# Optimization experiments

Measured on AMD Instinct MI355X. Metric: run time of the kernel, lower is better.

Reference implementation:

```python
import jax, jax.numpy as jnp
import numpy as np


def setup_inputs() -> dict:
    key = jax.random.key(0)
    ks = jax.random.split(key, 8)
    B, C, H, W, D = 2, 128, 16, 16, 16
    C8 = C // 8
    return {
        "x": jax.random.normal(ks[0], (B, C, H, W, D), dtype=jnp.float32),
        "wq": jax.random.normal(ks[1], (C8, C), dtype=jnp.float32) * (1.0 / np.sqrt(C)),
        "bq": jax.random.normal(ks[2], (C8,), dtype=jnp.float32) * 0.02,
        "wk": jax.random.normal(ks[3], (C8, C), dtype=jnp.float32) * (1.0 / np.sqrt(C)),
        "bk": jax.random.normal(ks[4], (C8,), dtype=jnp.float32) * 0.02,
        "wv": jax.random.normal(ks[5], (C, C), dtype=jnp.float32) * (1.0 / np.sqrt(C)),
        "bv": jax.random.normal(ks[6], (C,), dtype=jnp.float32) * 0.02,
        "gamma": jax.random.normal(ks[7], (1,), dtype=jnp.float32) * 0.1,
    }


def reference(x, wq, bq, wk, bk, wv, bv, gamma):
    B, C, H, W, D = x.shape
    N = H * W * D
    xf = x.reshape(B, C, N)                      # (B, C, N) flatten H,W,D
    # 1x1x1 convs == per-voxel linear over channels
    q = jnp.einsum('oc,bcn->bon', wq, xf) + bq[None, :, None]   # (B, C//8, N)
    k = jnp.einsum('oc,bcn->bon', wk, xf) + bk[None, :, None]   # (B, C//8, N)
    v = jnp.einsum('oc,bcn->bon', wv, xf) + bv[None, :, None]   # (B, C, N)
    # energy[b, i, j] = sum_c q[b,c,i] * k[b,c,j]  (no scaling, as in source)
    energy = jnp.einsum('bci,bcj->bij', q, k)                   # (B, N, N)
    attn = jax.nn.softmax(energy, axis=-1)
    # out[b,c,i] = sum_j v[b,c,j] * attn[b,i,j]
    out = jnp.einsum('bcj,bij->bci', v, attn)                   # (B, C, N)
    out = out.reshape(B, C, H, W, D)
    return gamma[0] * out + x
```

## Files before the change

kernel.cpp:

```cpp
#include <hip/hip_runtime.h>
#include <hip/hip_bf16.h>
#include <math.h>

#define N_VOX 4096
#define LOG2E 1.44269504f

typedef __bf16 bf16x4 __attribute__((ext_vector_type(4)));
typedef __bf16 bf16x8 __attribute__((ext_vector_type(8)));
typedef float f32x4 __attribute__((ext_vector_type(4)));
typedef float f32x16 __attribute__((ext_vector_type(16)));

#define QT_OFF 0
#define KT_OFF 262144
#define VP_OFF 524288

__device__ __forceinline__ f32x16 mfma32_bf16(bf16x8 a, bf16x8 b, f32x16 c) {
  return __builtin_amdgcn_mfma_f32_32x32x16_bf16(a, b, c, 0, 0, 0);
}
__device__ __forceinline__ f32x16 mfma32_fp8(long a, long b, f32x16 c) {
  return __builtin_amdgcn_mfma_f32_32x32x16_fp8_fp8(a, b, c, 0, 0, 0);
}
__device__ __forceinline__ void pinl(long& v) { asm volatile("" : "+v"(v)); }
__device__ __forceinline__ void pinb(bf16x8& v) { asm volatile("" : "+v"(v)); }

__device__ __forceinline__ unsigned f32_to_fp8x4(float a, float b, float c, float d) {
  int v = __builtin_amdgcn_cvt_pk_fp8_f32(a, b, 0, false);
  v = __builtin_amdgcn_cvt_pk_fp8_f32(c, d, v, true);
  return (unsigned)v;
}
__device__ __forceinline__ unsigned char f32_to_fp8(float a) {
  return (unsigned char)(__builtin_amdgcn_cvt_pk_fp8_f32(a, a, 0, false) & 0xff);
}

__global__ __launch_bounds__(256) void proj_kernel(
    const float* __restrict__ x,
    const float* __restrict__ wq, const float* __restrict__ bq,
    const float* __restrict__ wk, const float* __restrict__ bk,
    const float* __restrict__ wv, const float* __restrict__ bv,
    unsigned char* __restrict__ ws8) {
  __shared__ __bf16 xs[32 * 136];
  __shared__ __bf16 wb[160 * 136];

  const int t   = threadIdx.x;
  const int bid = blockIdx.x;
  const int b   = bid >> 7;
  const int n0  = (bid & 127) * 32;

  for (int i = t; i < 5120; i += 256) {
    int gid = i * 4;
    const float* src = (gid < 2048) ? wq + gid
                     : (gid < 4096) ? wk + (gid - 2048)
                                    : wv + (gid - 4096);
    float4 f = *reinterpret_cast<const float4*>(src);
    int r = gid >> 7, col = gid & 127;
    bf16x4 o;
    o[0] = (__bf16)f.x; o[1] = (__bf16)f.y; o[2] = (__bf16)f.z; o[3] = (__bf16)f.w;
    *reinterpret_cast<bf16x4*>(&wb[r * 136 + col]) = o;
  }
  for (int idx = t; idx < 128 * 8; idx += 256) {
    int c = idx >> 3, v4 = idx & 7;
    float4 xv = *reinterpret_cast<const float4*>(
        x + (size_t)(b * 128 + c) * N_VOX + n0 + v4 * 4);
    xs[(v4 * 4 + 0) * 136 + c] = (__bf16)xv.x;
    xs[(v4 * 4 + 1) * 136 + c] = (__bf16)xv.y;
    xs[(v4 * 4 + 2) * 136 + c] = (__bf16)xv.z;
    xs[(v4 * 4 + 3) * 136 + c] = (__bf16)xv.w;
  }
  __syncthreads();

  const int w = t >> 6, lane = t & 63;
  const int cq = lane & 15, g = lane >> 4, g8 = g * 8, g4 = g * 4;

  __bf16* qt = reinterpret_cast<__bf16*>(ws8 + QT_OFF);
  __bf16* kt = reinterpret_cast<__bf16*>(ws8 + KT_OFF);
  unsigned char* vp = ws8 + VP_OFF;
  const f32x4 zero4 = {0.f, 0.f, 0.f, 0.f};

  for (int ot = w; ot < 10; ot += 4) {
    int wrow = (ot == 0) ? cq : (ot == 1) ? 16 + cq : 32 + (ot - 2) * 16 + cq;
    const float* bias = (ot == 0) ? bq : (ot == 1) ? bk : bv + (ot - 2) * 16;

    f32x4 acc[2] = {zero4, zero4};
#pragma unroll
    for (int ks = 0; ks < 4; ++ks) {
      bf16x8 af = *reinterpret_cast<const bf16x8*>(&wb[wrow * 136 + ks * 32 + g8]);
#pragma unroll
      for (int nf = 0; nf < 2; ++nf) {
        bf16x8 bfr = *reinterpret_cast<const bf16x8*>(
            &xs[(nf * 16 + cq) * 136 + ks * 32 + g8]);
        acc[nf] = __builtin_amdgcn_mfma_f32_16x16x32_bf16(af, bfr, acc[nf], 0, 0, 0);
      }
    }

    float4 bl = *reinterpret_cast<const float4*>(bias + g4);
    const float* blp = reinterpret_cast<const float*>(&bl);
#pragma unroll
    for (int nf = 0; nf < 2; ++nf) {
      int n = n0 + nf * 16 + cq;
      if (ot < 2) {
        bf16x4 pk;
#pragma unroll
        for (int v = 0; v < 4; ++v) {
          float val = acc[nf][v] + blp[v];
          pk[v] = (__bf16)((ot == 0) ? val * LOG2E : val);
        }
        __bf16* dst = (ot == 0) ? qt : kt;
        *reinterpret_cast<bf16x4*>(dst + (size_t)(b * 4096 + n) * 16 + g4) = pk;
      } else {
#pragma unroll
        for (int v = 0; v < 4; ++v) {
          float val = acc[nf][v] + blp[v];
          int c = (ot - 2) * 16 + g4 + v;
          vp[(((size_t)(b * 256 + (n >> 4)) * 2 + (c >> 6)) << 10)
             + (((((n >> 3) & 1) << 5) | (c & 31)) * 16)
             + ((c >> 5) & 1) * 8 + (n & 7)] = f32_to_fp8(val);
        }
      }
    }
  }
}

__global__ __launch_bounds__(512, 2) void attn_kernel(
    const unsigned char* __restrict__ ws8,
    const float* __restrict__ x,
    const float* __restrict__ gamma_p,
    float* __restrict__ out) {
  __shared__ float o_lds[4][128][33];
  __shared__ float m_lds[8][32], l_lds[8][32], lstar_lds[32];

  const int t    = threadIdx.x;
  const int w    = t >> 6;
  const int lane = t & 63;
  const int l31  = lane & 31;
  const int hi   = lane >> 5;

  const int raw = blockIdx.x;
  const int xcd = raw & 7;
  const int b   = xcd >> 2;
  const int qt0 = ((raw >> 3) * 4 + (xcd & 3)) * 32;

  const __bf16* qt = reinterpret_cast<const __bf16*>(ws8 + QT_OFF);
  const __bf16* kt = reinterpret_cast<const __bf16*>(ws8 + KT_OFF);
  const unsigned char* vp = ws8 + VP_OFF;

  bf16x8 qf = *reinterpret_cast<const bf16x8*>(
      qt + (size_t)(b * 4096 + qt0 + l31) * 16 + hi * 8);

  f32x16 acc[4];
#pragma unroll
  for (int cb = 0; cb < 4; ++cb)
#pragma unroll
    for (int r = 0; r < 16; ++r) acc[cb][r] = 0.f;
  const f32x16 zero16 = acc[0];
  float m = -1e30f, l = 0.f;

  const __bf16* kbase = kt + (size_t)(b * 4096 + l31) * 16 + hi * 8;
  const unsigned char* vbase = vp + (size_t)b * 524288 + lane * 16;

  const int jt_base = w * 8;

  bf16x8 kf0 = *reinterpret_cast<const bf16x8*>(kbase + (size_t)(jt_base * 64) * 16);
  bf16x8 kf1 = *reinterpret_cast<const bf16x8*>(kbase + (size_t)(jt_base * 64 + 32) * 16);

#pragma unroll 1
  for (int tile = 0; tile < 8; ++tile) {
    const int jt = jt_base + tile;
    const int jtn = jt_base + ((tile + 1) & 7);

    long vf[4][4];
#pragma unroll
    for (int jc = 0; jc < 4; ++jc)
#pragma unroll
      for (int ch = 0; ch < 2; ++ch) {
        long2 L = *reinterpret_cast<const long2*>(
            vbase + (((size_t)(jt * 4 + jc) * 2 + ch) << 10));
        vf[jc][2 * ch] = L.x; vf[jc][2 * ch + 1] = L.y;
      }
    bf16x8 kn0 = *reinterpret_cast<const bf16x8*>(kbase + (size_t)(jtn * 64) * 16);
    bf16x8 kn1 = *reinterpret_cast<const bf16x8*>(kbase + (size_t)(jtn * 64 + 32) * 16);

    f32x16 sf0 = mfma32_bf16(kf0, qf, zero16);
    f32x16 sf1 = mfma32_bf16(kf1, qf, zero16);

    float tmax = sf0[0];
#pragma unroll
    for (int r = 1; r < 16; ++r) tmax = fmaxf(tmax, sf0[r]);
#pragma unroll
    for (int r = 0; r < 16; ++r) tmax = fmaxf(tmax, sf1[r]);
    tmax = fmaxf(tmax, __shfl_xor(tmax, 32));

    if (__any(tmax > m + 8.0f)) {
      float mn = fmaxf(m, tmax);
      float sc = exp2f(m - mn);
#pragma unroll
      for (int cb = 0; cb < 4; ++cb)
#pragma unroll
        for (int r = 0; r < 16; ++r) acc[cb][r] *= sc;
      l *= sc;
      m = mn;
    }

    float psum = 0.f;
    unsigned W0[4], W1[4], X0[4], X1[4];
#pragma unroll
    for (int i = 0; i < 4; ++i) {
      float a = exp2f(sf0[4 * i] - m),     bb = exp2f(sf0[4 * i + 1] - m);
      float c = exp2f(sf0[4 * i + 2] - m), d  = exp2f(sf0[4 * i + 3] - m);
      psum += (a + bb) + (c + d);
      W0[i] = f32_to_fp8x4(a, bb, c, d);
    }
#pragma unroll
    for (int i = 0; i < 4; ++i) {
      float a = exp2f(sf1[4 * i] - m),     bb = exp2f(sf1[4 * i + 1] - m);
      float c = exp2f(sf1[4 * i + 2] - m), d  = exp2f(sf1[4 * i + 3] - m);
      psum += (a + bb) + (c + d);
      W1[i] = f32_to_fp8x4(a, bb, c, d);
    }
    psum += __shfl_xor(psum, 32);
    l += psum;

#pragma unroll
    for (int i = 0; i < 4; ++i) {
      X0[i] = __shfl_xor(W0[i], 32);
      X1[i] = __shfl_xor(W1[i], 32);
    }

#pragma unroll
    for (int jc = 0; jc < 4; ++jc)
#pragma unroll
      for (int cb = 0; cb < 4; ++cb) pinl(vf[jc][cb]);
    pinb(kn0); pinb(kn1);

    __builtin_amdgcn_s_setprio(1);
#pragma unroll
    for (int jc = 0; jc < 4; ++jc) {
      const int pb = (jc & 1) * 2;
      unsigned wd0, wd1;
      if (jc < 2) {
        wd0 = hi ? X0[pb + 1] : W0[pb];
        wd1 = hi ? W0[pb + 1] : X0[pb];
      } else {
        wd0 = hi ? X1[pb + 1] : W1[pb];
        wd1 = hi ? W1[pb + 1] : X1[pb];
      }
      long pf = (long)(((unsigned long long)wd1 << 32) | wd0);
#pragma unroll
      for (int cb = 0; cb < 4; ++cb)
        acc[cb] = mfma32_fp8(vf[jc][cb], pf, acc[cb]);
    }
    __builtin_amdgcn_s_setprio(0);

    kf0 = kn0; kf1 = kn1;
  }

  if (lane < 32) { m_lds[w][lane] = m; l_lds[w][lane] = l; }
  __syncthreads();

  float mstar = m_lds[0][l31];
#pragma unroll
  for (int ww = 1; ww < 8; ++ww) mstar = fmaxf(mstar, m_lds[ww][l31]);
  float lstar = 0.f;
#pragma unroll
  for (int ww = 0; ww < 8; ++ww)
    lstar += l_lds[ww][l31] * exp2f(m_lds[ww][l31] - mstar);
  float sc = exp2f(m - mstar);
  if (w == 0 && lane < 32) lstar_lds[lane] = lstar;

  const int rr = w & 3;
  if (w < 4) {
#pragma unroll
    for (int cb = 0; cb < 4; ++cb)
#pragma unroll
      for (int r = 0; r < 16; ++r)
        o_lds[rr][cb * 32 + (r & 3) + 8 * (r >> 2) + 4 * hi][l31] = acc[cb][r] * sc;
  }
  __syncthreads();
  if (w >= 4) {
#pragma unroll
    for (int cb = 0; cb < 4; ++cb)
#pragma unroll
      for (int r = 0; r < 16; ++r)
        o_lds[rr][cb * 32 + (r & 3) + 8 * (r >> 2) + 4 * hi][l31] += acc[cb][r] * sc;
  }
  __syncthreads();

  const float g0 = gamma_p[0];
  for (int idx = t; idx < 128 * 32; idx += 512) {
    int c = idx >> 5, qq = idx & 31;
    float o = (o_lds[0][c][qq] + o_lds[1][c][qq] +
               o_lds[2][c][qq] + o_lds[3][c][qq]) / lstar_lds[qq];
    size_t addr = (size_t)(b * 128 + c) * N_VOX + qt0 + qq;
    out[addr] = fmaf(g0, o, x[addr]);
  }
}

extern "C" void kernel_launch(void* const* d_in, const int* in_sizes, int n_in,
                              void* d_out, int out_size, void* d_ws, size_t ws_size,
                              hipStream_t stream) {
  const float* x     = (const float*)d_in[0];
  const float* wq    = (const float*)d_in[1];
  const float* bq    = (const float*)d_in[2];
  const float* wk    = (const float*)d_in[3];
  const float* bk    = (const float*)d_in[4];
  const float* wv    = (const float*)d_in[5];
  const float* bv    = (const float*)d_in[6];
  const float* gamma = (const float*)d_in[7];
  float* out = (float*)d_out;
  unsigned char* ws8 = (unsigned char*)d_ws;

  proj_kernel<<<256, 256, 0, stream>>>(x, wq, bq, wk, bk, wv, bv, ws8);
  attn_kernel<<<256, 512, 0, stream>>>(ws8, x, gamma, out);
}
```

Measured before the change: 32.02 us.

## Fuse projection and attention into one cooperative kernel with grid sync

Merges the projection kernel and the attention kernel into a single cooperative launch that runs the projection, issues a grid-wide barrier, and then runs attention. Each block's Q tile stays in shared memory instead of making a round trip through global workspace, and the LDS buffer is reused between the two phases. The aim is to drop the second kernel launch gap and the Q store/load, at the cost of a grid sync and a requirement that all 256 blocks be co-resident.

```diff
diff --git a/kernel.cpp b/kernel.cpp
--- a/kernel.cpp
+++ b/kernel.cpp
@@ -1,6 +1,9 @@
 #include <hip/hip_runtime.h>
 #include <hip/hip_bf16.h>
+#include <hip/hip_cooperative_groups.h>
 #include <math.h>
+
+namespace cg = cooperative_groups;
 
 #define N_VOX 4096
 #define LOG2E 1.44269504f
@@ -10,9 +13,8 @@
 typedef float f32x4 __attribute__((ext_vector_type(4)));
 typedef float f32x16 __attribute__((ext_vector_type(16)));
 
-#define QT_OFF 0
-#define KT_OFF 262144
-#define VP_OFF 524288
+#define KT_OFF 0
+#define VP_OFF 262144
 
 __device__ __forceinline__ f32x16 mfma32_bf16(bf16x8 a, bf16x8 b, f32x16 c) {
   return __builtin_amdgcn_mfma_f32_32x32x16_bf16(a, b, c, 0, 0, 0);
@@ -32,119 +34,114 @@
   return (unsigned char)(__builtin_amdgcn_cvt_pk_fp8_f32(a, a, 0, false) & 0xff);
 }
 
-__global__ __launch_bounds__(256) void proj_kernel(
+__global__ __launch_bounds__(512, 2) void fused_kernel(
     const float* __restrict__ x,
     const float* __restrict__ wq, const float* __restrict__ bq,
     const float* __restrict__ wk, const float* __restrict__ bk,
     const float* __restrict__ wv, const float* __restrict__ bv,
+    const float* __restrict__ gamma_p,
+    float* __restrict__ out,
     unsigned char* __restrict__ ws8) {
-  __shared__ __bf16 xs[32 * 136];
-  __shared__ __bf16 wb[160 * 136];
-
-  const int t   = threadIdx.x;
-  const int bid = blockIdx.x;
-  const int b   = bid >> 7;
-  const int n0  = (bid & 127) * 32;
-
-  for (int i = t; i < 5120; i += 256) {
-    int gid = i * 4;
-    const float* src = (gid < 2048) ? wq + gid
-                     : (gid < 4096) ? wk + (gid - 2048)
-                                    : wv + (gid - 4096);
-    float4 f = *reinterpret_cast<const float4*>(src);
-    int r = gid >> 7, col = gid & 127;
-    bf16x4 o;
-    o[0] = (__bf16)f.x; o[1] = (__bf16)f.y; o[2] = (__bf16)f.z; o[3] = (__bf16)f.w;
-    *reinterpret_cast<bf16x4*>(&wb[r * 136 + col]) = o;
-  }
-  for (int idx = t; idx < 128 * 8; idx += 256) {
-    int c = idx >> 3, v4 = idx & 7;
-    float4 xv = *reinterpret_cast<const float4*>(
-        x + (size_t)(b * 128 + c) * N_VOX + n0 + v4 * 4);
-    xs[(v4 * 4 + 0) * 136 + c] = (__bf16)xv.x;
-    xs[(v4 * 4 + 1) * 136 + c] = (__bf16)xv.y;
-    xs[(v4 * 4 + 2) * 136 + c] = (__bf16)xv.z;
-    xs[(v4 * 4 + 3) * 136 + c] = (__bf16)xv.w;
-  }
-  __syncthreads();
-
-  const int w = t >> 6, lane = t & 63;
-  const int cq = lane & 15, g = lane >> 4, g8 = g * 8, g4 = g * 4;
-
-  __bf16* qt = reinterpret_cast<__bf16*>(ws8 + QT_OFF);
-  __bf16* kt = reinterpret_cast<__bf16*>(ws8 + KT_OFF);
-  unsigned char* vp = ws8 + VP_OFF;
-  const f32x4 zero4 = {0.f, 0.f, 0.f, 0.f};
-
-  for (int ot = w; ot < 10; ot += 4) {
-    int wrow = (ot == 0) ? cq : (ot == 1) ? 16 + cq : 32 + (ot - 2) * 16 + cq;
-    const float* bias = (ot == 0) ? bq : (ot == 1) ? bk : bv + (ot - 2) * 16;
-
-    f32x4 acc[2] = {zero4, zero4};
-#pragma unroll
-    for (int ks = 0; ks < 4; ++ks) {
-      bf16x8 af = *reinterpret_cast<const bf16x8*>(&wb[wrow * 136 + ks * 32 + g8]);
-#pragma unroll
-      for (int nf = 0; nf < 2; ++nf) {
-        bf16x8 bfr = *reinterpret_cast<const bf16x8*>(
-            &xs[(nf * 16 + cq) * 136 + ks * 32 + g8]);
-        acc[nf] = __builtin_amdgcn_mfma_f32_16x16x32_bf16(af, bfr, acc[nf], 0, 0, 0);
-      }
-    }
-
-    float4 bl = *reinterpret_cast<const float4*>(bias + g4);
-    const float* blp = reinterpret_cast<const float*>(&bl);
-#pragma unroll
-    for (int nf = 0; nf < 2; ++nf) {
-      int n = n0 + nf * 16 + cq;
-      if (ot < 2) {
-        bf16x4 pk;
-#pragma unroll
-        for (int v = 0; v < 4; ++v) {
-          float val = acc[nf][v] + blp[v];
-          pk[v] = (__bf16)((ot == 0) ? val * LOG2E : val);
-        }
-        __bf16* dst = (ot == 0) ? qt : kt;
-        *reinterpret_cast<bf16x4*>(dst + (size_t)(b * 4096 + n) * 16 + g4) = pk;
-      } else {
-#pragma unroll
-        for (int v = 0; v < 4; ++v) {
-          float val = acc[nf][v] + blp[v];
-          int c = (ot - 2) * 16 + g4 + v;
-          vp[(((size_t)(b * 256 + (n >> 4)) * 2 + (c >> 6)) << 10)
-             + (((((n >> 3) & 1) << 5) | (c & 31)) * 16)
-             + ((c >> 5) & 1) * 8 + (n & 7)] = f32_to_fp8(val);
-        }
-      }
-    }
-  }
-}
-
-__global__ __launch_bounds__(512, 2) void attn_kernel(
-    const unsigned char* __restrict__ ws8,
-    const float* __restrict__ x,
-    const float* __restrict__ gamma_p,
-    float* __restrict__ out) {
-  __shared__ float o_lds[4][128][33];
+  __shared__ __align__(16) unsigned char smem[67584];
+  __shared__ __align__(16) __bf16 q_lds[32 * 16];
   __shared__ float m_lds[8][32], l_lds[8][32], lstar_lds[32];
 
   const int t    = threadIdx.x;
   const int w    = t >> 6;
   const int lane = t & 63;
-  const int l31  = lane & 31;
-  const int hi   = lane >> 5;
 
   const int raw = blockIdx.x;
   const int xcd = raw & 7;
   const int b   = xcd >> 2;
-  const int qt0 = ((raw >> 3) * 4 + (xcd & 3)) * 32;
-
-  const __bf16* qt = reinterpret_cast<const __bf16*>(ws8 + QT_OFF);
-  const __bf16* kt = reinterpret_cast<const __bf16*>(ws8 + KT_OFF);
-  const unsigned char* vp = ws8 + VP_OFF;
-
-  bf16x8 qf = *reinterpret_cast<const bf16x8*>(
-      qt + (size_t)(b * 4096 + qt0 + l31) * 16 + hi * 8);
+  const int n0  = ((raw >> 3) * 4 + (xcd & 3)) * 32;
+
+  __bf16* kt = reinterpret_cast<__bf16*>(ws8 + KT_OFF);
+  unsigned char* vp = ws8 + VP_OFF;
+
+  {
+    __bf16* xs = reinterpret_cast<__bf16*>(smem);
+    __bf16* wb = reinterpret_cast<__bf16*>(smem + 8704);
+
+    for (int i = t; i < 5120; i += 512) {
+      int gid = i * 4;
+      const float* src = (gid < 2048) ? wq + gid
+                       : (gid < 4096) ? wk + (gid - 2048)
+                                      : wv + (gid - 4096);
+      float4 f = *reinterpret_cast<const float4*>(src);
+      int r = gid >> 7, col = gid & 127;
+      bf16x4 o;
+      o[0] = (__bf16)f.x; o[1] = (__bf16)f.y; o[2] = (__bf16)f.z; o[3] = (__bf16)f.w;
+      *reinterpret_cast<bf16x4*>(&wb[r * 136 + col]) = o;
+    }
+    for (int idx = t; idx < 128 * 8; idx += 512) {
+      int c = idx >> 3, v4 = idx & 7;
+      float4 xv = *reinterpret_cast<const float4*>(
+          x + (size_t)(b * 128 + c) * N_VOX + n0 + v4 * 4);
+      xs[(v4 * 4 + 0) * 136 + c] = (__bf16)xv.x;
+      xs[(v4 * 4 + 1) * 136 + c] = (__bf16)xv.y;
+      xs[(v4 * 4 + 2) * 136 + c] = (__bf16)xv.z;
+      xs[(v4 * 4 + 3) * 136 + c] = (__bf16)xv.w;
+    }
+    __syncthreads();
+
+    const int cq = lane & 15, g = lane >> 4, g8 = g * 8, g4 = g * 4;
+    const f32x4 zero4 = {0.f, 0.f, 0.f, 0.f};
+
+    for (int ot = w; ot < 10; ot += 8) {
+      int wrow = (ot == 0) ? cq : (ot == 1) ? 16 + cq : 32 + (ot - 2) * 16 + cq;
+      const float* bias = (ot == 0) ? bq : (ot == 1) ? bk : bv + (ot - 2) * 16;
+
+      f32x4 acc[2] = {zero4, zero4};
+#pragma unroll
+      for (int ks = 0; ks < 4; ++ks) {
+        bf16x8 af = *reinterpret_cast<const bf16x8*>(&wb[wrow * 136 + ks * 32 + g8]);
+#pragma unroll
+        for (int nf = 0; nf < 2; ++nf) {
+          bf16x8 bfr = *reinterpret_cast<const bf16x8*>(
+              &xs[(nf * 16 + cq) * 136 + ks * 32 + g8]);
+          acc[nf] = __builtin_amdgcn_mfma_f32_16x16x32_bf16(af, bfr, acc[nf], 0, 0, 0);
+        }
+      }
+
+      float4 bl = *reinterpret_cast<const float4*>(bias + g4);
+      const float* blp = reinterpret_cast<const float*>(&bl);
+#pragma unroll
+      for (int nf = 0; nf < 2; ++nf) {
+        int n = n0 + nf * 16 + cq;
+        if (ot == 0) {
+          bf16x4 pk;
+#pragma unroll
+          for (int v = 0; v < 4; ++v) pk[v] = (__bf16)((acc[nf][v] + blp[v]) * LOG2E);
+          *reinterpret_cast<bf16x4*>(&q_lds[(nf * 16 + cq) * 16 + g4]) = pk;
+        } else if (ot == 1) {
+          bf16x4 pk;
+#pragma unroll
+          for (int v = 0; v < 4; ++v) pk[v] = (__bf16)(acc[nf][v] + blp[v]);
+          *reinterpret_cast<bf16x4*>(kt + (size_t)(b * 4096 + n) * 16 + g4) = pk;
+        } else {
+#pragma unroll
+          for (int v = 0; v < 4; ++v) {
+            float val = acc[nf][v] + blp[v];
+            int c = (ot - 2) * 16 + g4 + v;
+            vp[(((size_t)(b * 256 + (n >> 4)) * 2 + (c >> 6)) << 10)
+               + (((((n >> 3) & 1) << 5) | (c & 31)) * 16)
+               + ((c >> 5) & 1) * 8 + (n & 7)] = f32_to_fp8(val);
+          }
+        }
+      }
+    }
+  }
+
+  __threadfence();
+  cg::this_grid().sync();
+
+  float (*o_lds)[128][33] = reinterpret_cast<float (*)[128][33]>(smem);
+
+  const int l31 = lane & 31;
+  const int hi  = lane >> 5;
+  const int qt0 = n0;
+
+  bf16x8 qf = *reinterpret_cast<const bf16x8*>(&q_lds[l31 * 16 + hi * 8]);
 
   f32x16 acc[4];
 #pragma unroll
@@ -308,6 +305,8 @@
   float* out = (float*)d_out;
   unsigned char* ws8 = (unsigned char*)d_ws;
 
-  proj_kernel<<<256, 256, 0, stream>>>(x, wq, bq, wk, bk, wv, bv, ws8);
-  attn_kernel<<<256, 512, 0, stream>>>(ws8, x, gamma, out);
-}
+  void* args[] = {(void*)&x, (void*)&wq, (void*)&bq, (void*)&wk, (void*)&bk,
+                  (void*)&wv, (void*)&bv, (void*)&gamma, (void*)&out, (void*)&ws8};
+  hipLaunchCooperativeKernel((const void*)fused_kernel, dim3(256), dim3(512),
+                             args, 0, stream);
+}
```

After: 121.6 us. 3.8x slower.
